# Performance work log

Measured on AMD Instinct MI355X. Metric: run time of the kernel, lower is better.

## Reference

```python
import jax, jax.numpy as jnp
import numpy as np

B, C, G, K, S, P, R = 4, 256, 16, 7, 1, 3, 4
H = W = 56


def setup_inputs() -> dict:
    key = jax.random.key(0)
    k1, k2, k3 = jax.random.split(key, 3)
    x = jax.random.normal(k1, (B, C, H, W), jnp.float32)
    reduce_w = jax.random.normal(k2, (C // R, C), jnp.float32) * 0.05
    reduce_b = jnp.zeros((C // R,), jnp.float32)
    span_w = jax.random.normal(k3, (K * K * G, C // R), jnp.float32) * 0.05
    span_b = jnp.zeros((K * K * G,), jnp.float32)
    return {"x": x, "reduce_w": reduce_w, "reduce_b": reduce_b,
            "span_w": span_w, "span_b": span_b}


def reference(x, reduce_w, reduce_b, span_w, span_b):
    b, c, h_in, w_in = x.shape
    Ho = (h_in + 2 * P - K) // S + 1
    Wo = (w_in + 2 * P - K) // S + 1
    # im2col patches, channel ordering (C, kh, kw) — matches torch.nn.Unfold
    patches = jax.lax.conv_general_dilated_patches(
        x, (K, K), (S, S), [(P, P), (P, P)])  # (B, C*K*K, Ho, Wo)
    patches = patches.reshape(b, G, c // G, K * K, Ho, Wo)
    # kernel generation branch: AvgPool(s) (identity for s=1) -> 1x1 reduce -> 1x1 span
    if S > 1:
        xk = jax.lax.reduce_window(x, 0.0, jax.lax.add,
                                   (1, 1, S, S), (1, 1, S, S), 'VALID') / (S * S)
    else:
        xk = x
    h = jnp.einsum('bchw,oc->bohw', xk, reduce_w) + reduce_b[None, :, None, None]
    kern = jnp.einsum('bchw,oc->bohw', h, span_w) + span_b[None, :, None, None]
    kern = kern.reshape(b, G, 1, K * K, Ho, Wo)
    # dynamic per-pixel depthwise-style multiply-reduce over the K*K window
    out = (kern * patches).sum(axis=3)  # (B, G, C//G, Ho, Wo)
    return out.reshape(b, c, Ho, Wo)
```

## Files before the change

### kernel.cpp

```cpp
#include <hip/hip_runtime.h>
#include <hip/hip_fp16.h>
#include <stdint.h>

#define HH   56
#define WW   56
#define HWP  3136
#define CC   256
#define GG   16
#define CGR  16
#define KT   7
#define KK   49
#define TH   2
#define XROW 32
#define XPL  260
#define PBLK 512
#define NPB  196
#define H2SB (4 * NPB * PBLK * 4)

typedef _Float16 h2_t   __attribute__((ext_vector_type(2)));
typedef __fp16   fp16x2 __attribute__((ext_vector_type(2)));
typedef _Float16 v8h    __attribute__((ext_vector_type(8)));
typedef float    v4f    __attribute__((ext_vector_type(4)));
union pk32 { uint32_t u; h2_t h; __half2 hh; fp16x2 f; };
union frag { uint32_t u[4]; v8h h; };

static __device__ __forceinline__ uint32_t pkrtz(float a, float b) {
    pk32 p; p.f = __builtin_amdgcn_cvt_pkrtz(a, b); return p.u;
}

static __device__ __forceinline__ frag pack_afrag(const float* rowp, int quad) {
    frag a;
    const float4 p0 = *(const float4*)&rowp[quad * 8];
    const float4 p1 = *(const float4*)&rowp[quad * 8 + 4];
    a.u[0] = pkrtz(p0.x, p0.y); a.u[1] = pkrtz(p0.z, p0.w);
    a.u[2] = pkrtz(p1.x, p1.y); a.u[3] = pkrtz(p1.z, p1.w);
    return a;
}

__global__ __launch_bounds__(256)
void gemm1_mfma(const float* __restrict__ rw, const float* __restrict__ rb,
                const float* __restrict__ x, uint32_t* __restrict__ h2s,
                uint16_t* __restrict__ xf)
{
    const int b = blockIdx.z, px0 = blockIdx.x * 32;
    const int t = threadIdx.x;
    const int wave = t >> 6, lane = t & 63, quad = lane >> 4, n16 = lane & 15;

    __shared__ __align__(16) uint32_t ldsB[2][1024];

    const int px = t & 31;
    const int q4 = t >> 5;
    const float* xb = x + (size_t)b * CC * HWP + px0 + px;

    float r[4][8];
#pragma unroll
    for (int k = 0; k < 4; ++k)
#pragma unroll
        for (int cc = 0; cc < 8; ++cc)
            r[k][cc] = xb[(size_t)(k * 64 + q4 * 8 + cc) * HWP];

    const float* rwr = rw + (size_t)(wave * 16 + n16) * CC;
    frag af0[4], af1[4];
#pragma unroll
    for (int k = 0; k < 4; ++k) {
        af0[k] = pack_afrag(rwr + k * 64, quad);
        af1[k] = pack_afrag(rwr + k * 64 + 32, quad);
    }

    {
        uint4 w;
        w.x = pkrtz(r[0][0], r[0][1]); w.y = pkrtz(r[0][2], r[0][3]);
        w.z = pkrtz(r[0][4], r[0][5]); w.w = pkrtz(r[0][6], r[0][7]);
        *(uint4*)&ldsB[0][q4 * 128 + px * 4] = w;
    }
    __syncthreads();

    v4f acc[2];
    acc[0] = v4f{0.f,0.f,0.f,0.f}; acc[1] = v4f{0.f,0.f,0.f,0.f};
#pragma unroll
    for (int k = 0; k < 4; ++k) {
        if (k < 3) {
            uint4 w;
            w.x = pkrtz(r[k+1][0], r[k+1][1]); w.y = pkrtz(r[k+1][2], r[k+1][3]);
            w.z = pkrtz(r[k+1][4], r[k+1][5]); w.w = pkrtz(r[k+1][6], r[k+1][7]);
            *(uint4*)&ldsB[(k + 1) & 1][q4 * 128 + px * 4] = w;
        }
        const uint32_t* B = ldsB[k & 1];
#pragma unroll
        for (int nt = 0; nt < 2; ++nt) {
            frag b0, b1;
            *(uint4*)b0.u = *(const uint4*)&B[quad * 128 + (nt * 16 + n16) * 4];
            *(uint4*)b1.u = *(const uint4*)&B[(4 + quad) * 128 + (nt * 16 + n16) * 4];
            acc[nt] = __builtin_amdgcn_mfma_f32_16x16x32_f16(af0[k].h, b0.h, acc[nt], 0, 0, 0);
            acc[nt] = __builtin_amdgcn_mfma_f32_16x16x32_f16(af1[k].h, b1.h, acc[nt], 0, 0, 0);
        }
        __syncthreads();
    }

    {
        uint16_t* xfp = xf + (size_t)b * CC * HWP + px0 + px;
#pragma unroll
        for (int k = 0; k < 4; ++k)
#pragma unroll
            for (int cc = 0; cc < 8; ++cc) {
                pk32 p; p.f = __builtin_amdgcn_cvt_pkrtz(r[k][cc], r[k][cc]);
                xfp[(size_t)(k * 64 + q4 * 8 + cc) * HWP] = (uint16_t)p.u;
            }
    }

    uint32_t* ldsT = &ldsB[0][0];
#pragma unroll
    for (int nt = 0; nt < 2; ++nt)
#pragma unroll
        for (int pr = 0; pr < 2; ++pr) {
            const int cp = wave * 8 + quad * 2 + pr;
            ldsT[cp * 33 + nt * 16 + n16] =
                pkrtz(acc[nt][2 * pr] + rb[2 * cp], acc[nt][2 * pr + 1] + rb[2 * cp + 1]);
        }
    __syncthreads();
    {
        const int oq4 = t >> 5, px32 = t & 31;
        uint4 w;
        w.x = ldsT[(oq4 * 4 + 0) * 33 + px32];
        w.y = ldsT[(oq4 * 4 + 1) * 33 + px32];
        w.z = ldsT[(oq4 * 4 + 2) * 33 + px32];
        w.w = ldsT[(oq4 * 4 + 3) * 33 + px32];
        uint32_t* hp = h2s + (size_t)b * NPB * PBLK
                     + (size_t)(blockIdx.x * 2 + (px32 >> 4)) * PBLK
                     + oq4 * 64 + (px32 & 15) * 4;
        *(uint4*)hp = w;
    }
}

__global__ __launch_bounds__(256, 5)
void invol_fused(const uint16_t* __restrict__ xf, const uint32_t* __restrict__ h2s,
                 const float* __restrict__ sw, const float* __restrict__ sb,
                 float* __restrict__ out)
{
    const int h0 = blockIdx.x * TH, g = blockIdx.y, b = blockIdx.z;

    __shared__ __align__(16) uint32_t sXh[16 * XPL];
    __shared__ __align__(16) uint32_t sK[KK * 56];

    const int t = threadIdx.x;
    const int wave = t >> 6, lane = t & 63, quad = lane >> 4, n16 = lane & 15;

    const int mt0 = wave * 16 + n16;
    const int mtap = mt0 > 48 ? 48 : mt0;
    const float* swr = sw + (size_t)(g * KK + mtap) * 64;
    const frag a0 = pack_afrag(swr, quad);
    const frag a1 = pack_afrag(swr + 32, quad);

    float bvv[4];
#pragma unroll
    for (int reg = 0; reg < 4; ++reg) {
        const int tp = wave * 16 + quad * 4 + reg;
        bvv[reg] = (tp < KK) ? sb[g * KK + tp] : 0.f;
    }

    {
        const int ch = t >> 4, rr = (t >> 1) & 7, side = t & 1;
        uint2 z; z.x = 0; z.y = 0;
        *(uint2*)&sXh[ch * XPL + rr * XROW + (side ? 30 : 0)] = z;
    }
    {
        const uint16_t* xb = xf + (size_t)(b * CC + g * CGR) * HWP;
#pragma unroll
        for (int k = 0; k < 4; ++k) {
            const int i = t + 256 * k;
            if (i < 896) {
                const int u4 = i % 7, row = i / 7;
                const int ch = row >> 3, rr = row & 7;
                const int hh = h0 - 3 + rr;
                uint4 v; v.x = 0; v.y = 0; v.z = 0; v.w = 0;
                if (hh >= 0 && hh < HH)
                    v = *(const uint4*)&xb[(size_t)ch * HWP + hh * WW + 8 * u4];
                uint32_t* d = &sXh[ch * XPL + rr * XROW + 2 + 4 * u4];
                uint2 p0; p0.x = v.x; p0.y = v.y;
                uint2 p1; p1.x = v.z; p1.y = v.w;
                *(uint2*)&d[0] = p0;
                *(uint2*)&d[2] = p1;
            }
        }
    }

    {
        const uint32_t* hb = h2s + (size_t)b * NPB * PBLK + (size_t)(blockIdx.x * 7) * PBLK;
        v4f acc[7];
#pragma unroll
        for (int nt = 0; nt < 7; ++nt) acc[nt] = v4f{0.f,0.f,0.f,0.f};
#pragma unroll
        for (int nt = 0; nt < 7; ++nt) {
            const uint32_t* pb = hb + nt * PBLK + n16 * 4;
            frag b0, b1;
            *(uint4*)b0.u = *(const uint4*)&pb[quad * 64];
            *(uint4*)b1.u = *(const uint4*)&pb[(4 + quad) * 64];
            acc[nt] = __builtin_amdgcn_mfma_f32_16x16x32_f16(a0.h, b0.h, acc[nt], 0, 0, 0);
            acc[nt] = __builtin_amdgcn_mfma_f32_16x16x32_f16(a1.h, b1.h, acc[nt], 0, 0, 0);
        }
        _Float16* sKh = (_Float16*)sK;
#pragma unroll
        for (int nt = 0; nt < 7; ++nt) {
            const int px = nt * 16 + n16;
#pragma unroll
            for (int reg = 0; reg < 4; ++reg) {
                const int tp = wave * 16 + quad * 4 + reg;
                if (tp < KK) sKh[tp * 112 + px] = (_Float16)(acc[nt][reg] + bvv[reg]);
            }
        }
    }
    __syncthreads();

    if (t < 224) {
        const int ch = t & 15, q = t >> 4, r = q & 1, wq = q >> 1;
        const uint32_t* xpl = &sXh[ch * XPL + 4 * wq];
        float o0=0,o1=0,o2=0,o3=0,o4=0,o5=0,o6=0,o7=0;
#pragma unroll
        for (int kh = 0; kh < KT; ++kh) {
            const int rr = r + kh;
            uint32_t E[8];
            *(uint4*)&E[0] = *(const uint4*)&xpl[rr * XROW];
            *(uint4*)&E[4] = *(const uint4*)&xpl[rr * XROW + 4];
            uint32_t O[7];
#pragma unroll
            for (int j = 0; j < 7; ++j) O[j] = __builtin_amdgcn_alignbit(E[j + 1], E[j], 16);
            pk32 va0, va1, va2, va3;
            va0.u = va1.u = va2.u = va3.u = 0;
            const uint32_t* kq = &sK[(kh * KT) * 56 + r * 28 + 4 * wq];
#pragma unroll
            for (int kw = 0; kw < KT; ++kw) {
                const uint4 kk = *(const uint4*)&kq[kw * 56];
                pk32 k0, k1, k2, k3; k0.u = kk.x; k1.u = kk.y; k2.u = kk.z; k3.u = kk.w;
                pk32 s0, s1, s2, s3;
                if (kw & 1) {
                    const int e = (kw + 1) >> 1;
                    s0.u = E[e]; s1.u = E[e + 1]; s2.u = E[e + 2]; s3.u = E[e + 3];
                } else {
                    const int oI = kw >> 1;
                    s0.u = O[oI]; s1.u = O[oI + 1]; s2.u = O[oI + 2]; s3.u = O[oI + 3];
                }
                va0.hh = __hfma2(k0.hh, s0.hh, va0.hh);
                va1.hh = __hfma2(k1.hh, s1.hh, va1.hh);
                va2.hh = __hfma2(k2.hh, s2.hh, va2.hh);
                va3.hh = __hfma2(k3.hh, s3.hh, va3.hh);
            }
            const float2 f0 = __half22float2(va0.hh); o0 += f0.x; o1 += f0.y;
            const float2 f1 = __half22float2(va1.hh); o2 += f1.x; o3 += f1.y;
            const float2 f2 = __half22float2(va2.hh); o4 += f2.x; o5 += f2.y;
            const float2 f3 = __half22float2(va3.hh); o6 += f3.x; o7 += f3.y;
        }
        float* op = out + (size_t)(b * CC + g * CGR + ch) * HWP + (h0 + r) * WW + 8 * wq;
        *(float4*)&op[0] = make_float4(o0, o1, o2, o3);
        *(float4*)&op[4] = make_float4(o4, o5, o6, o7);
    }
}

extern "C" void kernel_launch(void* const* d_in, const int* in_sizes, int n_in,
                              void* d_out, int out_size, void* d_ws, size_t ws_size,
                              hipStream_t stream)
{
    const float* x  = (const float*)d_in[0];
    const float* rw = (const float*)d_in[1];
    const float* rb = (const float*)d_in[2];
    const float* sw = (const float*)d_in[3];
    const float* sb = (const float*)d_in[4];
    float* out  = (float*)d_out;

    uint32_t* h2s = (uint32_t*)d_ws;
    uint16_t* xf  = (uint16_t*)((char*)d_ws + H2SB);

    gemm1_mfma<<<dim3(HWP / 32, 1, 4), 256, 0, stream>>>(rw, rb, x, h2s, xf);
    invol_fused<<<dim3(HH / TH, GG, 4), 256, 0, stream>>>(xf, h2s, sw, sb, out);
}
```

Baseline: 93.86 us.

## Shrink gemm1 tiles to 16 pixels with 128-thread blocks for more parallelism

```diff
diff --git a/kernel.cpp b/kernel.cpp
--- a/kernel.cpp
+++ b/kernel.cpp
@@ -37,19 +37,19 @@
     return a;
 }
 
-__global__ __launch_bounds__(256)
+__global__ __launch_bounds__(128)
 void gemm1_mfma(const float* __restrict__ rw, const float* __restrict__ rb,
                 const float* __restrict__ x, uint32_t* __restrict__ h2s,
                 uint16_t* __restrict__ xf)
 {
-    const int b = blockIdx.z, px0 = blockIdx.x * 32;
+    const int b = blockIdx.z, px0 = blockIdx.x * 16;
     const int t = threadIdx.x;
     const int wave = t >> 6, lane = t & 63, quad = lane >> 4, n16 = lane & 15;
 
-    __shared__ __align__(16) uint32_t ldsB[2][1024];
-
-    const int px = t & 31;
-    const int q4 = t >> 5;
+    __shared__ __align__(16) uint32_t ldsB[2][512];
+
+    const int px = t & 15;
+    const int q4 = t >> 4;
     const float* xb = x + (size_t)b * CC * HWP + px0 + px;
 
     float r[4][8];
@@ -59,19 +59,22 @@
         for (int cc = 0; cc < 8; ++cc)
             r[k][cc] = xb[(size_t)(k * 64 + q4 * 8 + cc) * HWP];
 
-    const float* rwr = rw + (size_t)(wave * 16 + n16) * CC;
-    frag af0[4], af1[4];
-#pragma unroll
-    for (int k = 0; k < 4; ++k) {
-        af0[k] = pack_afrag(rwr + k * 64, quad);
-        af1[k] = pack_afrag(rwr + k * 64 + 32, quad);
+    frag af0[2][4], af1[2][4];
+#pragma unroll
+    for (int m = 0; m < 2; ++m) {
+        const float* rwr = rw + (size_t)((wave * 2 + m) * 16 + n16) * CC;
+#pragma unroll
+        for (int k = 0; k < 4; ++k) {
+            af0[m][k] = pack_afrag(rwr + k * 64, quad);
+            af1[m][k] = pack_afrag(rwr + k * 64 + 32, quad);
+        }
     }
 
     {
         uint4 w;
         w.x = pkrtz(r[0][0], r[0][1]); w.y = pkrtz(r[0][2], r[0][3]);
         w.z = pkrtz(r[0][4], r[0][5]); w.w = pkrtz(r[0][6], r[0][7]);
-        *(uint4*)&ldsB[0][q4 * 128 + px * 4] = w;
+        *(uint4*)&ldsB[0][q4 * 64 + px * 4] = w;
     }
     __syncthreads();
 
@@ -83,16 +86,16 @@
             uint4 w;
             w.x = pkrtz(r[k+1][0], r[k+1][1]); w.y = pkrtz(r[k+1][2], r[k+1][3]);
             w.z = pkrtz(r[k+1][4], r[k+1][5]); w.w = pkrtz(r[k+1][6], r[k+1][7]);
-            *(uint4*)&ldsB[(k + 1) & 1][q4 * 128 + px * 4] = w;
+            *(uint4*)&ldsB[(k + 1) & 1][q4 * 64 + px * 4] = w;
         }
         const uint32_t* B = ldsB[k & 1];
-#pragma unroll
-        for (int nt = 0; nt < 2; ++nt) {
-            frag b0, b1;
-            *(uint4*)b0.u = *(const uint4*)&B[quad * 128 + (nt * 16 + n16) * 4];
-            *(uint4*)b1.u = *(const uint4*)&B[(4 + quad) * 128 + (nt * 16 + n16) * 4];
-            acc[nt] = __builtin_amdgcn_mfma_f32_16x16x32_f16(af0[k].h, b0.h, acc[nt], 0, 0, 0);
-            acc[nt] = __builtin_amdgcn_mfma_f32_16x16x32_f16(af1[k].h, b1.h, acc[nt], 0, 0, 0);
+        frag b0, b1;
+        *(uint4*)b0.u = *(const uint4*)&B[quad * 64 + n16 * 4];
+        *(uint4*)b1.u = *(const uint4*)&B[(4 + quad) * 64 + n16 * 4];
+#pragma unroll
+        for (int m = 0; m < 2; ++m) {
+            acc[m] = __builtin_amdgcn_mfma_f32_16x16x32_f16(af0[m][k].h, b0.h, acc[m], 0, 0, 0);
+            acc[m] = __builtin_amdgcn_mfma_f32_16x16x32_f16(af1[m][k].h, b1.h, acc[m], 0, 0, 0);
         }
         __syncthreads();
     }
@@ -110,24 +113,24 @@
 
     uint32_t* ldsT = &ldsB[0][0];
 #pragma unroll
-    for (int nt = 0; nt < 2; ++nt)
+    for (int m = 0; m < 2; ++m)
 #pragma unroll
         for (int pr = 0; pr < 2; ++pr) {
-            const int cp = wave * 8 + quad * 2 + pr;
-            ldsT[cp * 33 + nt * 16 + n16] =
-                pkrtz(acc[nt][2 * pr] + rb[2 * cp], acc[nt][2 * pr + 1] + rb[2 * cp + 1]);
+            const int cp = (wave * 2 + m) * 8 + quad * 2 + pr;
+            ldsT[cp * 17 + n16] =
+                pkrtz(acc[m][2 * pr] + rb[2 * cp], acc[m][2 * pr + 1] + rb[2 * cp + 1]);
         }
     __syncthreads();
     {
-        const int oq4 = t >> 5, px32 = t & 31;
+        const int oq4 = t >> 4, px16 = t & 15;
         uint4 w;
-        w.x = ldsT[(oq4 * 4 + 0) * 33 + px32];
-        w.y = ldsT[(oq4 * 4 + 1) * 33 + px32];
-        w.z = ldsT[(oq4 * 4 + 2) * 33 + px32];
-        w.w = ldsT[(oq4 * 4 + 3) * 33 + px32];
+        w.x = ldsT[(oq4 * 4 + 0) * 17 + px16];
+        w.y = ldsT[(oq4 * 4 + 1) * 17 + px16];
+        w.z = ldsT[(oq4 * 4 + 2) * 17 + px16];
+        w.w = ldsT[(oq4 * 4 + 3) * 17 + px16];
         uint32_t* hp = h2s + (size_t)b * NPB * PBLK
-                     + (size_t)(blockIdx.x * 2 + (px32 >> 4)) * PBLK
-                     + oq4 * 64 + (px32 & 15) * 4;
+                     + (size_t)blockIdx.x * PBLK
+                     + oq4 * 64 + px16 * 4;
         *(uint4*)hp = w;
     }
 }
@@ -269,6 +272,6 @@
     uint32_t* h2s = (uint32_t*)d_ws;
     uint16_t* xf  = (uint16_t*)((char*)d_ws + H2SB);
 
-    gemm1_mfma<<<dim3(HWP / 32, 1, 4), 256, 0, stream>>>(rw, rb, x, h2s, xf);
+    gemm1_mfma<<<dim3(HWP / 16, 1, 4), 128, 0, stream>>>(rw, rb, x, h2s, xf);
     invol_fused<<<dim3(HH / TH, GG, 4), 256, 0, stream>>>(xf, h2s, sw, sb, out);
 }
```

After: 98.96 us. 5.4% more time.
